# Kernel optimization log

Hardware: AMD Instinct MI355X
Metric: run time of the kernel (lower is better)

The kernel has to match this reference:

```python
import jax, jax.numpy as jnp
import numpy as np

NUM_NODES = 50000
FEAT_DIM = 64
HIDDEN = 128
OUT_DIM = 128
NUM_EDGES = 640000


def setup_inputs() -> dict:
    key = jax.random.key(0)
    ks = jax.random.split(key, 8)
    edge_index = jax.random.randint(ks[0], (2, NUM_EDGES), 0, NUM_NODES, dtype=jnp.int32)
    emb = jax.random.normal(ks[1], (NUM_NODES, FEAT_DIM), dtype=jnp.float32) * 0.1
    # SAGEConv: lin_l (aggregated neighbors, with bias) and lin_r (root, no bias)
    s1 = 1.0 / np.sqrt(FEAT_DIM)
    W1l = jax.random.uniform(ks[2], (HIDDEN, FEAT_DIM), jnp.float32, -s1, s1)
    b1l = jnp.zeros((HIDDEN,), jnp.float32)
    W1r = jax.random.uniform(ks[3], (HIDDEN, FEAT_DIM), jnp.float32, -s1, s1)
    s2 = 1.0 / np.sqrt(HIDDEN)
    W2l = jax.random.uniform(ks[4], (OUT_DIM, HIDDEN), jnp.float32, -s2, s2)
    b2l = jnp.zeros((OUT_DIM,), jnp.float32)
    W2r = jax.random.uniform(ks[5], (OUT_DIM, HIDDEN), jnp.float32, -s2, s2)
    return {"edge_index": edge_index, "emb": emb, "W1l": W1l, "b1l": b1l,
            "W1r": W1r, "W2l": W2l, "b2l": b2l, "W2r": W2r}


def _sage_conv(x, src, dst, Wl, bl, Wr):
    # mean-aggregate source features at target nodes, then two linear paths
    msg = x[src]                                   # [E, d]
    agg = jax.ops.segment_sum(msg, dst, num_segments=NUM_NODES)
    deg = jax.ops.segment_sum(jnp.ones((src.shape[0],), x.dtype), dst,
                              num_segments=NUM_NODES)
    mean = agg / jnp.maximum(deg, 1.0)[:, None]    # [N, d]
    return mean @ Wl.T + bl + x @ Wr.T             # [N, out]


def reference(edge_index, emb, W1l, b1l, W1r, W2l, b2l, W2r):
    src, dst = edge_index[0], edge_index[1]
    h = jax.nn.relu(_sage_conv(emb, src, dst, W1l, b1l, W1r))
    return _sage_conv(h, src, dst, W2l, b2l, W2r)
```

## Files before the change

kernel.cpp:

```cpp
#include <hip/hip_runtime.h>

#define N_NODES 50000
#define FEAT    64
#define HID     128
#define N_EDGES 640000
#define NBLK    196
#define GCAP    64

typedef __attribute__((ext_vector_type(8))) short bf16x8;
typedef __attribute__((ext_vector_type(4))) float f32x4;

static __device__ __forceinline__ unsigned short f2bf(float f) {
    unsigned u = __float_as_uint(f);
    u = u + 0x7fffu + ((u >> 16) & 1u);
    return (unsigned short)(u >> 16);
}
static __device__ __forceinline__ float bflo(unsigned u) {
    return __uint_as_float(u << 16);
}
static __device__ __forceinline__ float bfhi(unsigned u) {
    return __uint_as_float(u & 0xffff0000u);
}

static __device__ __forceinline__ void gridbar(int* bar, int gen) {
    __syncthreads();
    if (threadIdx.x == 0) {
        __threadfence();
        int arrived = atomicAdd(&bar[0], 1);
        if (arrived == NBLK - 1) {
            atomicExch(&bar[0], 0);
            __threadfence();
            atomicExch(&bar[1], gen);
        } else {
            while (atomicAdd(&bar[1], 0) < gen) __builtin_amdgcn_s_sleep(2);
        }
        __threadfence();
    }
    __syncthreads();
}

__global__ __launch_bounds__(256) void histcvt_kernel(
        const int* __restrict__ dst, const float* __restrict__ emb,
        const float* __restrict__ W1l, const float* __restrict__ W1r,
        const float* __restrict__ W2l, const float* __restrict__ W2r,
        int* __restrict__ count, int* __restrict__ eslot,
        unsigned* __restrict__ emb_bf_u, unsigned* __restrict__ Wbf_u) {
    int gtid = blockIdx.x * 256 + threadIdx.x;
    if (gtid < N_EDGES) {
        int slot = atomicAdd(&count[dst[gtid]], 1);
        eslot[gtid] = slot;
    }
    for (int i = gtid; i < N_NODES * FEAT / 2; i += N_EDGES) {
        float2 v = ((const float2*)emb)[i];
        emb_bf_u[i] = ((unsigned)f2bf(v.y) << 16) | (unsigned)f2bf(v.x);
    }
    if (gtid < 24576) {
        int w = gtid * 2;
        float lo, hi;
        if (w < 8192)       { lo = W1l[w];         hi = W1l[w + 1]; }
        else if (w < 16384) { lo = W1r[w - 8192];  hi = W1r[w - 8191]; }
        else if (w < 32768) { lo = W2l[w - 16384]; hi = W2l[w - 16383]; }
        else                { lo = W2r[w - 32768]; hi = W2r[w - 32767]; }
        Wbf_u[gtid] = ((unsigned)f2bf(hi) << 16) | (unsigned)f2bf(lo);
    }
}

__global__ __launch_bounds__(256) void scanperm_kernel(
        const int* __restrict__ count, int* offset, int* dhist, int* dcur,
        int* bsum, int* boff, int* dstart, int* perm, int* bar) {
    __shared__ int tmp[256];
    __shared__ int lh[64];
    __shared__ int lb2[64];
    int t = threadIdx.x;
    int gtid = blockIdx.x * 256 + t;

    {
        if (t < 64) lh[t] = 0;
        int v = (gtid < N_NODES) ? count[gtid] : 0;
        tmp[t] = v;
        __syncthreads();
        if (gtid < N_NODES) atomicAdd(&lh[v < 63 ? v : 63], 1);
        for (int off = 1; off < 256; off <<= 1) {
            int add = (t >= off) ? tmp[t - off] : 0;
            __syncthreads();
            tmp[t] += add;
            __syncthreads();
        }
        if (gtid < N_NODES) offset[gtid] = tmp[t] - v;
        if (t == 255) bsum[blockIdx.x] = tmp[255];
        if (t < 64 && lh[t] > 0) atomicAdd(&dhist[t], lh[t]);
    }
    gridbar(bar, 1);

    if (blockIdx.x < 2) {
        const int* in  = (blockIdx.x == 0) ? bsum : dhist;
        int*       out = (blockIdx.x == 0) ? boff : dstart;
        int cnt        = (blockIdx.x == 0) ? NBLK : 64;
        int v = (t < cnt) ? in[t] : 0;
        tmp[t] = v;
        __syncthreads();
        for (int off = 1; off < 256; off <<= 1) {
            int add = (t >= off) ? tmp[t - off] : 0;
            __syncthreads();
            tmp[t] += add;
            __syncthreads();
        }
        if (t < cnt) out[t] = tmp[t] - v;
    }
    gridbar(bar, 2);

    if (gtid < N_NODES) offset[gtid] += boff[blockIdx.x];
    if (gtid == 0) offset[N_NODES] = N_EDGES;
    {
        if (t < 64) lh[t] = 0;
        __syncthreads();
        int d = 0, slot = 0;
        if (gtid < N_NODES) {
            int c = count[gtid];
            d = c < 63 ? c : 63;
            slot = atomicAdd(&lh[d], 1);
        }
        __syncthreads();
        if (t < 64 && lh[t] > 0) lb2[t] = atomicAdd(&dcur[t], lh[t]);
        __syncthreads();
        if (gtid < N_NODES) perm[dstart[d] + lb2[d] + slot] = gtid;
    }
}

__global__ void fill_kernel(const int* __restrict__ src, const int* __restrict__ dst,
                            const int* __restrict__ offset,
                            const int* __restrict__ eslot, int* __restrict__ esrc) {
    int e = blockIdx.x * blockDim.x + threadIdx.x;
    if (e >= N_EDGES) return;
    esrc[offset[dst[e]] + eslot[e]] = src[e];
}

__global__ __launch_bounds__(256) void fgemm1_kernel(
        const unsigned short* __restrict__ embb, const int* __restrict__ offset,
        const int* __restrict__ esrc, const int* __restrict__ perm,
        const short* __restrict__ Wl, const short* __restrict__ Wr,
        const float* __restrict__ bias, unsigned short* __restrict__ hout) {
    __shared__ unsigned short smean[16][72];
    __shared__ int sidx[16][GCAP];
    __shared__ int nid[16];
    int t = threadIdx.x;
    if (t < 16) nid[t] = perm[blockIdx.x * 16 + t];
    __syncthreads();

    int sub = t >> 4, fl = t & 15;
    int n = nid[sub];
    int beg = offset[n], deg = offset[n + 1] - beg;
    bool fast = deg <= GCAP;
    if (fast) { for (int j = fl; j < deg; j += 16) sidx[sub][j] = esrc[beg + j]; }
    float A0[4] = {0,0,0,0}, A1[4] = {0,0,0,0}, A2[4] = {0,0,0,0}, A3[4] = {0,0,0,0};
    const uint2* eb2 = (const uint2*)embb;
    {
        int i = 0;
        if (fast) {
            for (; i + 4 <= deg; i += 4) {
                uint2 v0 = eb2[(size_t)sidx[sub][i+0] * 16 + fl];
                uint2 v1 = eb2[(size_t)sidx[sub][i+1] * 16 + fl];
                uint2 v2 = eb2[(size_t)sidx[sub][i+2] * 16 + fl];
                uint2 v3 = eb2[(size_t)sidx[sub][i+3] * 16 + fl];
                A0[0]+=bflo(v0.x); A0[1]+=bfhi(v0.x); A0[2]+=bflo(v0.y); A0[3]+=bfhi(v0.y);
                A1[0]+=bflo(v1.x); A1[1]+=bfhi(v1.x); A1[2]+=bflo(v1.y); A1[3]+=bfhi(v1.y);
                A2[0]+=bflo(v2.x); A2[1]+=bfhi(v2.x); A2[2]+=bflo(v2.y); A2[3]+=bfhi(v2.y);
                A3[0]+=bflo(v3.x); A3[1]+=bfhi(v3.x); A3[2]+=bflo(v3.y); A3[3]+=bfhi(v3.y);
            }
            for (; i < deg; ++i) {
                uint2 v = eb2[(size_t)sidx[sub][i] * 16 + fl];
                A0[0]+=bflo(v.x); A0[1]+=bfhi(v.x); A0[2]+=bflo(v.y); A0[3]+=bfhi(v.y);
            }
        } else {
            for (; i < deg; ++i) {
                uint2 v = eb2[(size_t)esrc[beg + i] * 16 + fl];
                A0[0]+=bflo(v.x); A0[1]+=bfhi(v.x); A0[2]+=bflo(v.y); A0[3]+=bfhi(v.y);
            }
        }
    }
    float dinv = 1.0f / fmaxf((float)deg, 1.0f);
    float s0 = ((A0[0]+A1[0])+(A2[0]+A3[0])) * dinv;
    float s1 = ((A0[1]+A1[1])+(A2[1]+A3[1])) * dinv;
    float s2 = ((A0[2]+A1[2])+(A2[2]+A3[2])) * dinv;
    float s3 = ((A0[3]+A1[3])+(A2[3]+A3[3])) * dinv;
    uint2 o;
    o.x = ((unsigned)f2bf(s1) << 16) | (unsigned)f2bf(s0);
    o.y = ((unsigned)f2bf(s3) << 16) | (unsigned)f2bf(s2);
    *(uint2*)&smean[sub][fl * 4] = o;
    __syncthreads();

    int wave = t >> 6, lane = t & 63;
    int col = lane & 15, quad = lane >> 4;
    int ncol = nid[col];
    int nt0 = wave * 2, nt1 = nt0 + 1;
    f32x4 acc0 = (f32x4){0.f,0.f,0.f,0.f}, acc1 = (f32x4){0.f,0.f,0.f,0.f};
    #pragma unroll
    for (int kb = 0; kb < FEAT; kb += 32) {
        bf16x8 am = *(const bf16x8*)&smean[col][kb + quad * 8];
        bf16x8 ax = *(const bf16x8*)(embb + (size_t)ncol * FEAT + kb + quad * 8);
        bf16x8 bl0 = *(const bf16x8*)(Wl + (nt0 * 16 + col) * FEAT + kb + quad * 8);
        bf16x8 br0 = *(const bf16x8*)(Wr + (nt0 * 16 + col) * FEAT + kb + quad * 8);
        bf16x8 bl1 = *(const bf16x8*)(Wl + (nt1 * 16 + col) * FEAT + kb + quad * 8);
        bf16x8 br1 = *(const bf16x8*)(Wr + (nt1 * 16 + col) * FEAT + kb + quad * 8);
        acc0 = __builtin_amdgcn_mfma_f32_16x16x32_bf16(am, bl0, acc0, 0, 0, 0);
        acc0 = __builtin_amdgcn_mfma_f32_16x16x32_bf16(ax, br0, acc0, 0, 0, 0);
        acc1 = __builtin_amdgcn_mfma_f32_16x16x32_bf16(am, bl1, acc1, 0, 0, 0);
        acc1 = __builtin_amdgcn_mfma_f32_16x16x32_bf16(ax, br1, acc1, 0, 0, 0);
    }
    float bv0 = bias[nt0 * 16 + col];
    float bv1 = bias[nt1 * 16 + col];
    #pragma unroll
    for (int r = 0; r < 4; ++r) {
        int node = nid[quad * 4 + r];
        hout[(size_t)node * HID + nt0 * 16 + col] = f2bf(fmaxf(acc0[r] + bv0, 0.f));
        hout[(size_t)node * HID + nt1 * 16 + col] = f2bf(fmaxf(acc1[r] + bv1, 0.f));
    }
}

__global__ __launch_bounds__(256) void fgemm2_kernel(
        const unsigned short* __restrict__ hbf, const int* __restrict__ offset,
        const int* __restrict__ esrc, const int* __restrict__ perm,
        const short* __restrict__ Wl, const short* __restrict__ Wr,
        const float* __restrict__ bias, float* __restrict__ out) {
    __shared__ unsigned short smean[16][136];
    __shared__ int sidx[16][GCAP];
    __shared__ int nid[16];
    int t = threadIdx.x;
    if (t < 16) nid[t] = perm[blockIdx.x * 16 + t];
    __syncthreads();

    int sub = t >> 4, fl = t & 15;
    int n = nid[sub];
    int beg = offset[n], deg = offset[n + 1] - beg;
    bool fast = deg <= GCAP;
    if (fast) { for (int j = fl; j < deg; j += 16) sidx[sub][j] = esrc[beg + j]; }
    float A0[8] = {0,0,0,0,0,0,0,0}, A1[8] = {0,0,0,0,0,0,0,0};
    float A2[8] = {0,0,0,0,0,0,0,0}, A3[8] = {0,0,0,0,0,0,0,0};
    const uint4* hb4 = (const uint4*)hbf;
    #define ACCU(A, v) { \
        A[0]+=bflo((v).x); A[1]+=bfhi((v).x); A[2]+=bflo((v).y); A[3]+=bfhi((v).y); \
        A[4]+=bflo((v).z); A[5]+=bfhi((v).z); A[6]+=bflo((v).w); A[7]+=bfhi((v).w); }
    {
        int i = 0;
        if (fast) {
            for (; i + 4 <= deg; i += 4) {
                uint4 v0 = hb4[(size_t)sidx[sub][i+0] * 16 + fl];
                uint4 v1 = hb4[(size_t)sidx[sub][i+1] * 16 + fl];
                uint4 v2 = hb4[(size_t)sidx[sub][i+2] * 16 + fl];
                uint4 v3 = hb4[(size_t)sidx[sub][i+3] * 16 + fl];
                ACCU(A0, v0) ACCU(A1, v1) ACCU(A2, v2) ACCU(A3, v3)
            }
            for (; i < deg; ++i) {
                uint4 v = hb4[(size_t)sidx[sub][i] * 16 + fl];
                ACCU(A0, v)
            }
        } else {
            for (; i < deg; ++i) {
                uint4 v = hb4[(size_t)esrc[beg + i] * 16 + fl];
                ACCU(A0, v)
            }
        }
    }
    #undef ACCU
    float dinv = 1.0f / fmaxf((float)deg, 1.0f);
    unsigned ow[4];
    #pragma unroll
    for (int k = 0; k < 4; ++k) {
        float lo = ((A0[2*k]+A1[2*k])+(A2[2*k]+A3[2*k])) * dinv;
        float hi = ((A0[2*k+1]+A1[2*k+1])+(A2[2*k+1]+A3[2*k+1])) * dinv;
        ow[k] = ((unsigned)f2bf(hi) << 16) | (unsigned)f2bf(lo);
    }
    uint4 o4 = {ow[0], ow[1], ow[2], ow[3]};
    *(uint4*)&smean[sub][fl * 8] = o4;
    __syncthreads();

    int wave = t >> 6, lane = t & 63;
    int col = lane & 15, quad = lane >> 4;
    int ncol = nid[col];
    int nt0 = wave * 2, nt1 = nt0 + 1;
    f32x4 acc0 = (f32x4){0.f,0.f,0.f,0.f}, acc1 = (f32x4){0.f,0.f,0.f,0.f};
    #pragma unroll
    for (int kb = 0; kb < HID; kb += 32) {
        bf16x8 am = *(const bf16x8*)&smean[col][kb + quad * 8];
        bf16x8 ax = *(const bf16x8*)(hbf + (size_t)ncol * HID + kb + quad * 8);
        bf16x8 bl0 = *(const bf16x8*)(Wl + (nt0 * 16 + col) * HID + kb + quad * 8);
        bf16x8 br0 = *(const bf16x8*)(Wr + (nt0 * 16 + col) * HID + kb + quad * 8);
        bf16x8 bl1 = *(const bf16x8*)(Wl + (nt1 * 16 + col) * HID + kb + quad * 8);
        bf16x8 br1 = *(const bf16x8*)(Wr + (nt1 * 16 + col) * HID + kb + quad * 8);
        acc0 = __builtin_amdgcn_mfma_f32_16x16x32_bf16(am, bl0, acc0, 0, 0, 0);
        acc0 = __builtin_amdgcn_mfma_f32_16x16x32_bf16(ax, br0, acc0, 0, 0, 0);
        acc1 = __builtin_amdgcn_mfma_f32_16x16x32_bf16(am, bl1, acc1, 0, 0, 0);
        acc1 = __builtin_amdgcn_mfma_f32_16x16x32_bf16(ax, br1, acc1, 0, 0, 0);
    }
    float bv0 = bias[nt0 * 16 + col];
    float bv1 = bias[nt1 * 16 + col];
    #pragma unroll
    for (int r = 0; r < 4; ++r) {
        int node = nid[quad * 4 + r];
        out[(size_t)node * HID + nt0 * 16 + col] = acc0[r] + bv0;
        out[(size_t)node * HID + nt1 * 16 + col] = acc1[r] + bv1;
    }
}

extern "C" void kernel_launch(void* const* d_in, const int* in_sizes, int n_in,
                              void* d_out, int out_size, void* d_ws, size_t ws_size,
                              hipStream_t stream) {
    const int*   edge_index = (const int*)d_in[0];
    const float* emb        = (const float*)d_in[1];
    const float* W1l        = (const float*)d_in[2];
    const float* b1l        = (const float*)d_in[3];
    const float* W1r        = (const float*)d_in[4];
    const float* W2l        = (const float*)d_in[5];
    const float* b2l        = (const float*)d_in[6];
    const float* W2r        = (const float*)d_in[7];
    float* out = (float*)d_out;

    const int* src = edge_index;
    const int* dst = edge_index + N_EDGES;

    int* iws    = (int*)d_ws;
    int* offset = iws;
    int* count  = iws + 50004;
    int* dhist  = iws + 100004;
    int* dcur   = iws + 100068;
    int* bar    = iws + 100132;
    int* bsum   = iws + 100136;
    int* boff   = iws + 100392;
    int* dstart = iws + 100648;
    int* perm   = iws + 100712;
    int* esrc   = iws + 150712;
    int* eslot  = iws + 790712;
    unsigned short* W1l_bf = (unsigned short*)(iws + 1430712);
    unsigned short* W1r_bf = (unsigned short*)(iws + 1434808);
    unsigned short* W2l_bf = (unsigned short*)(iws + 1438904);
    unsigned short* W2r_bf = (unsigned short*)(iws + 1447096);
    unsigned short* Wbf    = W1l_bf;
    unsigned short* emb_bf = (unsigned short*)(iws + 1455288);
    unsigned short* hbf    = (unsigned short*)(iws + 3055288);

    (void)hipMemsetAsync(count, 0, (size_t)(100136 - 50004) * sizeof(int), stream);

    histcvt_kernel<<<(N_EDGES + 255) / 256, 256, 0, stream>>>(
        dst, emb, W1l, W1r, W2l, W2r, count, eslot,
        (unsigned*)emb_bf, (unsigned*)Wbf);
    scanperm_kernel<<<NBLK, 256, 0, stream>>>(
        count, offset, dhist, dcur, bsum, boff, dstart, perm, bar);
    fill_kernel<<<(N_EDGES + 255) / 256, 256, 0, stream>>>(
        src, dst, offset, eslot, esrc);

    fgemm1_kernel<<<N_NODES / 16, 256, 0, stream>>>(
        emb_bf, offset, esrc, perm,
        (const short*)W1l_bf, (const short*)W1r_bf, b1l, hbf);
    fgemm2_kernel<<<N_NODES / 16, 256, 0, stream>>>(
        hbf, offset, esrc, perm,
        (const short*)W2l_bf, (const short*)W2r_bf, b2l, out);
}
```

Baseline: 231.3 us.

## Pad gather lists with zero sentinel row and widen neighbor gather loads

Adds a zero-filled sentinel row after the bf16 embedding and hidden tables and pads each node's neighbor index list to a multiple of 16 or 8 with that sentinel. This lets the gather loops run fully unrolled 8-wide with no tail loop. Layer 1 now uses 16-byte loads split across two half-groups, combined with a shuffle. The change also reverses the degree-sorted node order so high-degree nodes are scheduled first, and requests 8 waves per SIMD in the launch bounds. Padding adds wasted loads for low-degree nodes, and the occupancy hint may cause register spills.

```diff
diff --git a/kernel.cpp b/kernel.cpp
--- a/kernel.cpp
+++ b/kernel.cpp
@@ -21,6 +21,12 @@
 static __device__ __forceinline__ float bfhi(unsigned u) {
     return __uint_as_float(u & 0xffff0000u);
 }
+
+#define ACC8(A, v) { \
+    A[0] += bflo((v).x); A[1] += bfhi((v).x); \
+    A[2] += bflo((v).y); A[3] += bfhi((v).y); \
+    A[4] += bflo((v).z); A[5] += bfhi((v).z); \
+    A[6] += bflo((v).w); A[7] += bfhi((v).w); }
 
 static __device__ __forceinline__ void gridbar(int* bar, int gen) {
     __syncthreads();
@@ -44,7 +50,8 @@
         const float* __restrict__ W1l, const float* __restrict__ W1r,
         const float* __restrict__ W2l, const float* __restrict__ W2r,
         int* __restrict__ count, int* __restrict__ eslot,
-        unsigned* __restrict__ emb_bf_u, unsigned* __restrict__ Wbf_u) {
+        unsigned* __restrict__ emb_bf_u, unsigned* __restrict__ Wbf_u,
+        unsigned* __restrict__ hbf_u) {
     int gtid = blockIdx.x * 256 + threadIdx.x;
     if (gtid < N_EDGES) {
         int slot = atomicAdd(&count[dst[gtid]], 1);
@@ -54,6 +61,8 @@
         float2 v = ((const float2*)emb)[i];
         emb_bf_u[i] = ((unsigned)f2bf(v.y) << 16) | (unsigned)f2bf(v.x);
     }
+    if (gtid < FEAT / 2) emb_bf_u[N_NODES * FEAT / 2 + gtid] = 0u;
+    if (gtid < HID / 2)  hbf_u[N_NODES * HID / 2 + gtid]   = 0u;
     if (gtid < 24576) {
         int w = gtid * 2;
         float lo, hi;
@@ -123,7 +132,8 @@
         __syncthreads();
         if (t < 64 && lh[t] > 0) lb2[t] = atomicAdd(&dcur[t], lh[t]);
         __syncthreads();
-        if (gtid < N_NODES) perm[dstart[d] + lb2[d] + slot] = gtid;
+        if (gtid < N_NODES)
+            perm[(N_NODES - 1) - (dstart[d] + lb2[d] + slot)] = gtid;
     }
 }
 
@@ -135,7 +145,7 @@
     esrc[offset[dst[e]] + eslot[e]] = src[e];
 }
 
-__global__ __launch_bounds__(256) void fgemm1_kernel(
+__global__ __launch_bounds__(256, 8) void fgemm1_kernel(
         const unsigned short* __restrict__ embb, const int* __restrict__ offset,
         const int* __restrict__ esrc, const int* __restrict__ perm,
         const short* __restrict__ Wl, const short* __restrict__ Wr,
@@ -148,45 +158,48 @@
     __syncthreads();
 
     int sub = t >> 4, fl = t & 15;
+    int half = (t >> 3) & 1, fo = t & 7;
     int n = nid[sub];
     int beg = offset[n], deg = offset[n + 1] - beg;
     bool fast = deg <= GCAP;
-    if (fast) { for (int j = fl; j < deg; j += 16) sidx[sub][j] = esrc[beg + j]; }
-    float A0[4] = {0,0,0,0}, A1[4] = {0,0,0,0}, A2[4] = {0,0,0,0}, A3[4] = {0,0,0,0};
-    const uint2* eb2 = (const uint2*)embb;
-    {
-        int i = 0;
-        if (fast) {
-            for (; i + 4 <= deg; i += 4) {
-                uint2 v0 = eb2[(size_t)sidx[sub][i+0] * 16 + fl];
-                uint2 v1 = eb2[(size_t)sidx[sub][i+1] * 16 + fl];
-                uint2 v2 = eb2[(size_t)sidx[sub][i+2] * 16 + fl];
-                uint2 v3 = eb2[(size_t)sidx[sub][i+3] * 16 + fl];
-                A0[0]+=bflo(v0.x); A0[1]+=bfhi(v0.x); A0[2]+=bflo(v0.y); A0[3]+=bfhi(v0.y);
-                A1[0]+=bflo(v1.x); A1[1]+=bfhi(v1.x); A1[2]+=bflo(v1.y); A1[3]+=bfhi(v1.y);
-                A2[0]+=bflo(v2.x); A2[1]+=bfhi(v2.x); A2[2]+=bflo(v2.y); A2[3]+=bfhi(v2.y);
-                A3[0]+=bflo(v3.x); A3[1]+=bfhi(v3.x); A3[2]+=bflo(v3.y); A3[3]+=bfhi(v3.y);
-            }
-            for (; i < deg; ++i) {
-                uint2 v = eb2[(size_t)sidx[sub][i] * 16 + fl];
-                A0[0]+=bflo(v.x); A0[1]+=bfhi(v.x); A0[2]+=bflo(v.y); A0[3]+=bfhi(v.y);
-            }
-        } else {
-            for (; i < deg; ++i) {
-                uint2 v = eb2[(size_t)esrc[beg + i] * 16 + fl];
-                A0[0]+=bflo(v.x); A0[1]+=bfhi(v.x); A0[2]+=bflo(v.y); A0[3]+=bfhi(v.y);
-            }
+    int rr = (deg + 15) & ~15;
+    if (fast) {
+        for (int j = fl; j < rr; j += 16)
+            sidx[sub][j] = (j < deg) ? esrc[beg + j] : N_NODES;
+    }
+    float acc[8] = {0,0,0,0,0,0,0,0};
+    const uint4* eb4 = (const uint4*)embb;
+    if (fast) {
+        for (int i = 0; i < rr; i += 16) {
+            uint4 v0 = eb4[(size_t)sidx[sub][i +  0 + half] * 8 + fo];
+            uint4 v1 = eb4[(size_t)sidx[sub][i +  2 + half] * 8 + fo];
+            uint4 v2 = eb4[(size_t)sidx[sub][i +  4 + half] * 8 + fo];
+            uint4 v3 = eb4[(size_t)sidx[sub][i +  6 + half] * 8 + fo];
+            uint4 v4 = eb4[(size_t)sidx[sub][i +  8 + half] * 8 + fo];
+            uint4 v5 = eb4[(size_t)sidx[sub][i + 10 + half] * 8 + fo];
+            uint4 v6 = eb4[(size_t)sidx[sub][i + 12 + half] * 8 + fo];
+            uint4 v7 = eb4[(size_t)sidx[sub][i + 14 + half] * 8 + fo];
+            ACC8(acc, v0) ACC8(acc, v1) ACC8(acc, v2) ACC8(acc, v3)
+            ACC8(acc, v4) ACC8(acc, v5) ACC8(acc, v6) ACC8(acc, v7)
+        }
+    } else {
+        for (int i = half; i < deg; i += 2) {
+            uint4 v = eb4[(size_t)esrc[beg + i] * 8 + fo];
+            ACC8(acc, v)
         }
     }
     float dinv = 1.0f / fmaxf((float)deg, 1.0f);
-    float s0 = ((A0[0]+A1[0])+(A2[0]+A3[0])) * dinv;
-    float s1 = ((A0[1]+A1[1])+(A2[1]+A3[1])) * dinv;
-    float s2 = ((A0[2]+A1[2])+(A2[2]+A3[2])) * dinv;
-    float s3 = ((A0[3]+A1[3])+(A2[3]+A3[3])) * dinv;
-    uint2 o;
-    o.x = ((unsigned)f2bf(s1) << 16) | (unsigned)f2bf(s0);
-    o.y = ((unsigned)f2bf(s3) << 16) | (unsigned)f2bf(s2);
-    *(uint2*)&smean[sub][fl * 4] = o;
+    unsigned ow[4];
+    #pragma unroll
+    for (int k = 0; k < 4; ++k) {
+        float lo = acc[2 * k];     lo += __shfl_xor(lo, 8);
+        float hi = acc[2 * k + 1]; hi += __shfl_xor(hi, 8);
+        ow[k] = ((unsigned)f2bf(hi * dinv) << 16) | (unsigned)f2bf(lo * dinv);
+    }
+    if (half == 0) {
+        uint4 o4 = {ow[0], ow[1], ow[2], ow[3]};
+        *(uint4*)&smean[sub][fo * 8] = o4;
+    }
     __syncthreads();
 
     int wave = t >> 6, lane = t & 63;
@@ -217,7 +230,7 @@
     }
 }
 
-__global__ __launch_bounds__(256) void fgemm2_kernel(
+__global__ __launch_bounds__(256, 8) void fgemm2_kernel(
         const unsigned short* __restrict__ hbf, const int* __restrict__ offset,
         const int* __restrict__ esrc, const int* __restrict__ perm,
         const short* __restrict__ Wl, const short* __restrict__ Wr,
@@ -233,41 +246,38 @@
     int n = nid[sub];
     int beg = offset[n], deg = offset[n + 1] - beg;
     bool fast = deg <= GCAP;
-    if (fast) { for (int j = fl; j < deg; j += 16) sidx[sub][j] = esrc[beg + j]; }
-    float A0[8] = {0,0,0,0,0,0,0,0}, A1[8] = {0,0,0,0,0,0,0,0};
-    float A2[8] = {0,0,0,0,0,0,0,0}, A3[8] = {0,0,0,0,0,0,0,0};
+    int rr = (deg + 7) & ~7;
+    if (fast) {
+        for (int j = fl; j < rr; j += 16)
+            sidx[sub][j] = (j < deg) ? esrc[beg + j] : N_NODES;
+    }
+    float acc[8] = {0,0,0,0,0,0,0,0};
     const uint4* hb4 = (const uint4*)hbf;
-    #define ACCU(A, v) { \
-        A[0]+=bflo((v).x); A[1]+=bfhi((v).x); A[2]+=bflo((v).y); A[3]+=bfhi((v).y); \
-        A[4]+=bflo((v).z); A[5]+=bfhi((v).z); A[6]+=bflo((v).w); A[7]+=bfhi((v).w); }
-    {
-        int i = 0;
-        if (fast) {
-            for (; i + 4 <= deg; i += 4) {
-                uint4 v0 = hb4[(size_t)sidx[sub][i+0] * 16 + fl];
-                uint4 v1 = hb4[(size_t)sidx[sub][i+1] * 16 + fl];
-                uint4 v2 = hb4[(size_t)sidx[sub][i+2] * 16 + fl];
-                uint4 v3 = hb4[(size_t)sidx[sub][i+3] * 16 + fl];
-                ACCU(A0, v0) ACCU(A1, v1) ACCU(A2, v2) ACCU(A3, v3)
-            }
-            for (; i < deg; ++i) {
-                uint4 v = hb4[(size_t)sidx[sub][i] * 16 + fl];
-                ACCU(A0, v)
-            }
-        } else {
-            for (; i < deg; ++i) {
-                uint4 v = hb4[(size_t)esrc[beg + i] * 16 + fl];
-                ACCU(A0, v)
-            }
-        }
-    }
-    #undef ACCU
+    if (fast) {
+        for (int i = 0; i < rr; i += 8) {
+            uint4 v0 = hb4[(size_t)sidx[sub][i + 0] * 16 + fl];
+            uint4 v1 = hb4[(size_t)sidx[sub][i + 1] * 16 + fl];
+            uint4 v2 = hb4[(size_t)sidx[sub][i + 2] * 16 + fl];
+            uint4 v3 = hb4[(size_t)sidx[sub][i + 3] * 16 + fl];
+            uint4 v4 = hb4[(size_t)sidx[sub][i + 4] * 16 + fl];
+            uint4 v5 = hb4[(size_t)sidx[sub][i + 5] * 16 + fl];
+            uint4 v6 = hb4[(size_t)sidx[sub][i + 6] * 16 + fl];
+            uint4 v7 = hb4[(size_t)sidx[sub][i + 7] * 16 + fl];
+            ACC8(acc, v0) ACC8(acc, v1) ACC8(acc, v2) ACC8(acc, v3)
+            ACC8(acc, v4) ACC8(acc, v5) ACC8(acc, v6) ACC8(acc, v7)
+        }
+    } else {
+        for (int i = 0; i < deg; ++i) {
+            uint4 v = hb4[(size_t)esrc[beg + i] * 16 + fl];
+            ACC8(acc, v)
+        }
+    }
     float dinv = 1.0f / fmaxf((float)deg, 1.0f);
     unsigned ow[4];
     #pragma unroll
     for (int k = 0; k < 4; ++k) {
-        float lo = ((A0[2*k]+A1[2*k])+(A2[2*k]+A3[2*k])) * dinv;
-        float hi = ((A0[2*k+1]+A1[2*k+1])+(A2[2*k+1]+A3[2*k+1])) * dinv;
+        float lo = acc[2 * k] * dinv;
+        float hi = acc[2 * k + 1] * dinv;
         ow[k] = ((unsigned)f2bf(hi) << 16) | (unsigned)f2bf(lo);
     }
     uint4 o4 = {ow[0], ow[1], ow[2], ow[3]};
@@ -336,13 +346,13 @@
     unsigned short* W2r_bf = (unsigned short*)(iws + 1447096);
     unsigned short* Wbf    = W1l_bf;
     unsigned short* emb_bf = (unsigned short*)(iws + 1455288);
-    unsigned short* hbf    = (unsigned short*)(iws + 3055288);
+    unsigned short* hbf    = (unsigned short*)(iws + 3055320);
 
     (void)hipMemsetAsync(count, 0, (size_t)(100136 - 50004) * sizeof(int), stream);
 
     histcvt_kernel<<<(N_EDGES + 255) / 256, 256, 0, stream>>>(
         dst, emb, W1l, W1r, W2l, W2r, count, eslot,
-        (unsigned*)emb_bf, (unsigned*)Wbf);
+        (unsigned*)emb_bf, (unsigned*)Wbf, (unsigned*)hbf);
     scanperm_kernel<<<NBLK, 256, 0, stream>>>(
         count, offset, dhist, dcur, bsum, boff, dstart, perm, bar);
     fill_kernel<<<(N_EDGES + 255) / 256, 256, 0, stream>>>(
```

After: 274.9 us. 18.9% more time.
